# Performance work log

Hardware: AMD Instinct MI355X
Metric: run time of the kernel (lower is better)

Reference implementation:

```python
import jax, jax.numpy as jnp
import numpy as np

NUM_HEADS = 12
HEAD_DIM = 32  # all_head_size(384) / num_heads(12)


def setup_inputs() -> dict:
    key = jax.random.key(0)
    ks = jax.random.split(key, 8)
    B, Sq, Sk, Din, AH = 1, 4096, 4096, 768, 384
    scale = 1.0 / np.sqrt(Din)
    return {
        "hidden_states": jax.random.normal(ks[0], (B, Sq, Din), jnp.float32),
        "encoder_hidden_states": jax.random.normal(ks[1], (B, Sk, Din), jnp.float32),
        "encoder_attention_mask": jnp.zeros((B, 1, 1, Sk), jnp.float32),
        "Wq": jax.random.normal(ks[2], (Din, AH), jnp.float32) * scale,
        "bq": jnp.zeros((AH,), jnp.float32),
        "Wk": jax.random.normal(ks[3], (Din, AH), jnp.float32) * scale,
        "bk": jnp.zeros((AH,), jnp.float32),
        "Wv": jax.random.normal(ks[4], (Din, AH), jnp.float32) * scale,
        "bv": jnp.zeros((AH,), jnp.float32),
    }


def _split_heads(x):
    # [B, S, H*D] -> [B, H, S, D]
    B, S, _ = x.shape
    return x.reshape(B, S, NUM_HEADS, HEAD_DIM).transpose(0, 2, 1, 3)


def reference(hidden_states, encoder_hidden_states, encoder_attention_mask,
              Wq, bq, Wk, bk, Wv, bv):
    q = _split_heads(hidden_states @ Wq + bq)            # [B,H,Sq,D]
    k = _split_heads(encoder_hidden_states @ Wk + bk)    # [B,H,Sk,D]
    v = _split_heads(encoder_hidden_states @ Wv + bv)    # [B,H,Sk,D]

    scores = jnp.einsum('bhqd,bhkd->bhqk', q, k) / np.sqrt(HEAD_DIM)
    scores = scores + encoder_attention_mask              # additive mask, broadcast
    probs = jax.nn.softmax(scores, axis=-1)               # dropout is identity (eval)

    ctx = jnp.einsum('bhqk,bhkd->bhqd', probs, v)         # [B,H,Sq,D]
    B, H, Sq, D = ctx.shape
    return ctx.transpose(0, 2, 1, 3).reshape(B, Sq, H * D)  # [B,Sq,all_head_size]
```

## Files before the change

kernel.cpp:

```cpp
#include <hip/hip_runtime.h>
#include <hip/hip_bf16.h>

#define SQ 4096
#define SKK 4096
#define DIN 768
#define AHS 384
#define NHEAD 12
#define HD 32

typedef __attribute__((ext_vector_type(8))) short bf16x8;
typedef __attribute__((ext_vector_type(4))) float f32x4;
typedef __attribute__((ext_vector_type(4))) unsigned int u32x4;

#define LOG2E 1.4426950408889634f
#define QSCALE 0.25503486168652855f

#define GLD16(gp, lp) __builtin_amdgcn_global_load_lds( \
    (const __attribute__((address_space(1))) void*)(gp), \
    (__attribute__((address_space(3))) void*)(lp), 16, 0, 0)

__device__ __forceinline__ unsigned short bf16_rn(float x){
  unsigned int u = __float_as_uint(x);
  unsigned int r = u + 0x7fffu + ((u>>16)&1u);
  return (unsigned short)(r>>16);
}
__device__ __forceinline__ float bf16_f(unsigned short h){
  return __uint_as_float(((unsigned int)h)<<16);
}
__device__ __forceinline__ float fexp2(float x){
#if __has_builtin(__builtin_amdgcn_exp2f)
  return __builtin_amdgcn_exp2f(x);
#else
  float r; asm("v_exp_f32 %0, %1" : "=v"(r) : "v"(x)); return r;
#endif
}

__global__ void em_kernel(const float* __restrict__ mask, unsigned short* __restrict__ EMB){
  int idx = blockIdx.x*256 + threadIdx.x;
  if (idx < SKK) EMB[idx] = bf16_rn(__expf(mask[idx]));
}

__global__ __launch_bounds__(256) void prep2_kernel(
    const float* __restrict__ Wq, const float* __restrict__ Wk, const float* __restrict__ Wv,
    unsigned short* __restrict__ Wthi, unsigned short* __restrict__ Wtlo)
{
  const int z = blockIdx.z;
  const float* W = (z==0)?Wq:((z==1)?Wk:Wv);
  const int k0 = blockIdx.x*64, n0 = blockIdx.y*64;
  const int tid = threadIdx.x;

  __shared__ float T[64][65];

  const int kr = tid>>2, nc = (tid&3)*16;
  const float* src = W + (size_t)(k0+kr)*AHS + n0 + nc;
  #pragma unroll
  for (int p=0; p<4; ++p){
    f32x4 v = *(const f32x4*)(src + p*4);
    T[kr][nc + p*4 + 0] = v[0];
    T[kr][nc + p*4 + 1] = v[1];
    T[kr][nc + p*4 + 2] = v[2];
    T[kr][nc + p*4 + 3] = v[3];
  }
  __syncthreads();

  const int nr = tid>>2, ks = (tid&3)*16;
  unsigned short* dh = Wthi + (size_t)(z*AHS + n0 + nr)*DIN + k0 + ks;
  unsigned short* dl = Wtlo + (size_t)(z*AHS + n0 + nr)*DIN + k0 + ks;
  #pragma unroll
  for (int half=0; half<2; ++half){
    bf16x8 hv, lv;
    #pragma unroll
    for (int j=0; j<8; ++j){
      float v = T[ks + half*8 + j][nr];
      unsigned short hh = bf16_rn(v);
      hv[j] = (short)hh;
      lv[j] = (short)bf16_rn(v - bf16_f(hh));
    }
    *(bf16x8*)(dh + half*8) = hv;
    *(bf16x8*)(dl + half*8) = lv;
  }
}

__global__ __launch_bounds__(512,2) void proj5_kernel(
    const float* __restrict__ Xh, const float* __restrict__ Xe,
    const unsigned short* __restrict__ Wthi, const unsigned short* __restrict__ Wtlo,
    const float* __restrict__ bq, const float* __restrict__ bk, const float* __restrict__ bv,
    const unsigned short* __restrict__ EMB,
    unsigned short* __restrict__ Qhi, unsigned short* __restrict__ Qlo,
    unsigned short* __restrict__ Khi, unsigned short* __restrict__ Klo,
    unsigned short* __restrict__ Vt)
{
  const int bid = blockIdx.x;
  const int logical = (bid & 7)*36 + (bid >> 3);
  const int mb = logical & 31;
  const int rest = logical >> 5;
  const int nb = rest % 3, z = rest / 3;

  const float* A = (z==0) ? Xh : Xe;
  const unsigned short* Bh = Wthi + (size_t)z*(DIN*AHS);
  const unsigned short* Bl = Wtlo + (size_t)z*(DIN*AHS);
  const float* bias = (z==0) ? bq : ((z==1) ? bk : bv);

  const int m0 = mb*128;
  const int n0 = nb*128;
  const int tid = threadIdx.x;
  const int w = tid>>6, lane = tid&63;
  const int lm = lane&15, g = lane>>4;
  const int wm = w>>1, wn = w&1;

  __shared__ __align__(16) unsigned short SH[32768];

  const int srow = tid>>2, scn = tid&3;
  const int sidx = srow*32 + ((scn ^ ((srow>>1)&3))<<3);
  const float* pA = A + (size_t)(m0 + srow)*DIN + scn*8;
  const size_t gb = (size_t)(n0 + srow)*DIN + scn*8;

  f32x4 xa0, xa1; u32x4 rb, rlb;
  auto sload = [&](int kk){
    xa0 = *(const f32x4*)(pA + kk);
    xa1 = *(const f32x4*)(pA + kk + 4);
    rb  = *(const u32x4*)(Bh + gb + kk);
    if (z != 2) rlb = *(const u32x4*)(Bl + gb + kk);
  };
  auto swrite = [&](int b){
    float xx[8] = {xa0[0],xa0[1],xa0[2],xa0[3],xa1[0],xa1[1],xa1[2],xa1[3]};
    unsigned int hw[4];
    #pragma unroll
    for (int p=0;p<4;++p)
      asm("v_cvt_pk_bf16_f32 %0, %1, %2" : "=v"(hw[p]) : "v"(xx[2*p]), "v"(xx[2*p+1]));
    u32x4 ra = {hw[0],hw[1],hw[2],hw[3]};
    *(u32x4*)&SH[b*16384 + 0*4096 + sidx] = ra;
    *(u32x4*)&SH[b*16384 + 2*4096 + sidx] = rb;
    if (z != 2){
      unsigned int lw[4];
      #pragma unroll
      for (int p=0;p<4;++p){
        float h0 = __uint_as_float(hw[p]<<16);
        float h1 = __uint_as_float(hw[p] & 0xffff0000u);
        float l0 = xx[2*p] - h0, l1 = xx[2*p+1] - h1;
        asm("v_cvt_pk_bf16_f32 %0, %1, %2" : "=v"(lw[p]) : "v"(l0), "v"(l1));
      }
      u32x4 rla = {lw[0],lw[1],lw[2],lw[3]};
      *(u32x4*)&SH[b*16384 + 1*4096 + sidx] = rla;
      *(u32x4*)&SH[b*16384 + 3*4096 + sidx] = rlb;
    }
  };

  f32x4 acc[2][4];
  #pragma unroll
  for (int mi=0;mi<2;++mi)
    #pragma unroll
    for (int ni=0;ni<4;++ni) acc[mi][ni] = (f32x4){0.f,0.f,0.f,0.f};

  auto fidx = [&](int row)->int{ return row*32 + ((g ^ ((row>>1)&3))<<3); };

  sload(0); swrite(0); __syncthreads();
  int cur = 0;

  const int NKS = DIN/32;
  for (int t=0; t<NKS; ++t){
    if (t+1 < NKS) sload((t+1)*32);

    const unsigned short* AhL = &SH[cur*16384 + 0*4096];
    const unsigned short* AlL = &SH[cur*16384 + 1*4096];
    const unsigned short* BhL = &SH[cur*16384 + 2*4096];
    const unsigned short* BlL = &SH[cur*16384 + 3*4096];

    bf16x8 a0h = *(const bf16x8*)&AhL[fidx(wm*32 + lm)];
    bf16x8 a1h = *(const bf16x8*)&AhL[fidx(wm*32 + 16 + lm)];
    bf16x8 a0l, a1l;
    if (z != 2){
      a0l = *(const bf16x8*)&AlL[fidx(wm*32 + lm)];
      a1l = *(const bf16x8*)&AlL[fidx(wm*32 + 16 + lm)];
    }
    __builtin_amdgcn_s_setprio(1);
    #pragma unroll
    for (int ni=0; ni<4; ++ni){
      bf16x8 bh = *(const bf16x8*)&BhL[fidx(wn*64 + ni*16 + lm)];
      acc[0][ni] = __builtin_amdgcn_mfma_f32_16x16x32_bf16(a0h, bh, acc[0][ni], 0,0,0);
      acc[1][ni] = __builtin_amdgcn_mfma_f32_16x16x32_bf16(a1h, bh, acc[1][ni], 0,0,0);
      if (z != 2){
        bf16x8 bl = *(const bf16x8*)&BlL[fidx(wn*64 + ni*16 + lm)];
        acc[0][ni] = __builtin_amdgcn_mfma_f32_16x16x32_bf16(a0h, bl, acc[0][ni], 0,0,0);
        acc[1][ni] = __builtin_amdgcn_mfma_f32_16x16x32_bf16(a1h, bl, acc[1][ni], 0,0,0);
        acc[0][ni] = __builtin_amdgcn_mfma_f32_16x16x32_bf16(a0l, bh, acc[0][ni], 0,0,0);
        acc[1][ni] = __builtin_amdgcn_mfma_f32_16x16x32_bf16(a1l, bh, acc[1][ni], 0,0,0);
      }
    }
    __builtin_amdgcn_s_setprio(0);

    if (t+1 < NKS) swrite(cur^1);
    __syncthreads();
    cur ^= 1;
  }

  if (z != 2){
    #pragma unroll
    for (int ni=0; ni<4; ++ni){
      int col = n0 + wn*64 + ni*16 + lm;
      float bcol = bias[col];
      int hq = col>>5, d = col&31;
      #pragma unroll
      for (int mi=0; mi<2; ++mi){
        #pragma unroll
        for (int r=0; r<4; ++r){
          int row = m0 + wm*32 + mi*16 + g*4 + r;
          float v = acc[mi][ni][r] + bcol;
          if (z==0) v *= QSCALE;
          unsigned short hh = bf16_rn(v);
          unsigned short ll = bf16_rn(v - bf16_f(hh));
          size_t p = (z==0) ? ((size_t)hq*SQ + row)*HD + d
                            : ((size_t)hq*SKK + row)*HD + d;
          if (z==0){ Qhi[p]=hh; Qlo[p]=ll; } else { Khi[p]=hh; Klo[p]=ll; }
        }
      }
    }
  } else {
    #pragma unroll
    for (int ni=0; ni<4; ++ni){
      int lcol = wn*64 + ni*16 + lm;
      float bcol = bias[n0 + lcol];
      #pragma unroll
      for (int mi=0; mi<2; ++mi){
        #pragma unroll
        for (int r=0; r<4; ++r){
          int lrow = wm*32 + mi*16 + g*4 + r;
          float emf = bf16_f(EMB[m0 + lrow]);
          SH[lcol*128 + (lrow ^ ((lcol&7)<<3))] = bf16_rn((acc[mi][ni][r] + bcol) * emf);
        }
      }
    }
    __syncthreads();
    #pragma unroll
    for (int p=0; p<4; ++p){
      int c = tid>>2, rc = (tid&3)*8 + p*32;
      bf16x8 vv = *(const bf16x8*)&SH[c*128 + (rc ^ ((c&7)<<3))];
      *(bf16x8*)(Vt + (size_t)(n0 + c)*SKK + m0 + rc) = vv;
    }
  }
}

__global__ __launch_bounds__(256) void attn_kernel(
    const unsigned short* __restrict__ Qhi, const unsigned short* __restrict__ Qlo,
    const unsigned short* __restrict__ Khi, const unsigned short* __restrict__ Klo,
    const unsigned short* __restrict__ Vt, const unsigned short* __restrict__ EMB,
    float* __restrict__ opart, float* __restrict__ lpart,
    int nkt, int direct, int chunk)
{
  const int bid = blockIdx.x;
  const int logical = (bid & 7)*chunk + (bid >> 3);
  const int qt = logical & 63;
  const int rest = logical >> 6;
  const int h = rest % NHEAD, sp = rest / NHEAD;

  const int tid = threadIdx.x;
  const int w = tid>>6, lane = tid&63;
  const int lm = lane&15, g = lane>>4;
  const int qrow = qt*64 + w*16 + lm;
  const int kbeg = sp*nkt*64;

  __shared__ unsigned short KhL[2][2048];
  __shared__ unsigned short KlL[2][2048];
  __shared__ unsigned short VL [2][2048];

  const int krow_l = 16*w + (lane>>2);
  const int ksw_l = ((krow_l>>1)&1) ^ (((krow_l>>3)&1)<<1);
  const unsigned short* gKh = Khi + (size_t)h*SKK*HD
                            + (size_t)(kbeg + krow_l)*HD + (((lane&3)^ksw_l)<<3);
  const unsigned short* gKl = Klo + (size_t)h*SKK*HD
                            + (size_t)(kbeg + krow_l)*HD + (((lane&3)^ksw_l)<<3);
  const int vrow_l = 8*w + (lane>>3);
  const unsigned short* gV = Vt + (size_t)(h*HD + vrow_l)*SKK + kbeg
                           + (((lane&7)^(lane>>3))<<3);
  const unsigned short* pEM = EMB + kbeg + g*8;

  const int krs = ((lm>>2)<<3) + (lm&3);
  const int rsw = ((krs>>1)&1) ^ (((krs>>3)&1)<<1);
  const int kread0 = krs*32 + ((g ^ rsw)<<3);

  int vr[4];
  vr[0] = (lm*64      + g*8)      ^ ((lm&7)<<3);
  vr[1] = (lm*64      + 32 + g*8) ^ ((lm&7)<<3);
  vr[2] = ((lm+16)*64 + g*8)      ^ ((lm&7)<<3);
  vr[3] = ((lm+16)*64 + 32 + g*8) ^ ((lm&7)<<3);

  bf16x8 qh = *(const bf16x8*)(Qhi + ((size_t)h*SQ + qrow)*HD + g*8);
  bf16x8 ql = *(const bf16x8*)(Qlo + ((size_t)h*SQ + qrow)*HD + g*8);

  f32x4 o0 = {0.f,0.f,0.f,0.f}, o1 = {0.f,0.f,0.f,0.f};
  f32x4 lacc = {0.f,0.f,0.f,0.f};

  GLD16(gKh, &KhL[0][w*512]);
  GLD16(gKl, &KlL[0][w*512]);
  GLD16(gV,  &VL [0][w*512]);
  __syncthreads();

  #pragma unroll 2
  for (int t=0; t<nkt; ++t){
    const int cur = t&1;

    if (t+1 < nkt){
      gKh += 64*HD; gKl += 64*HD; gV += 64;
      GLD16(gKh, &KhL[cur^1][w*512]);
      GLD16(gKl, &KlL[cur^1][w*512]);
      GLD16(gV,  &VL [cur^1][w*512]);
    }

    bf16x8 em0 = *(const bf16x8*)(pEM);
    bf16x8 em1 = *(const bf16x8*)(pEM + 32);
    pEM += 64;

    unsigned int wds[8];
    #pragma unroll
    for (int ks=0; ks<4; ++ks){
      const int kidx = kread0 + (ks&1)*128 + (ks>>1)*1024;
      bf16x8 kh = *(const bf16x8*)(&KhL[cur][kidx]);
      bf16x8 kl = *(const bf16x8*)(&KlL[cur][kidx]);
      f32x4 a = {0.f,0.f,0.f,0.f};
      __builtin_amdgcn_s_setprio(1);
      a = __builtin_amdgcn_mfma_f32_16x16x32_bf16(kh, qh, a, 0,0,0);
      a = __builtin_amdgcn_mfma_f32_16x16x32_bf16(kh, ql, a, 0,0,0);
      a = __builtin_amdgcn_mfma_f32_16x16x32_bf16(kl, qh, a, 0,0,0);
      __builtin_amdgcn_s_setprio(0);
      float p0 = fexp2(a[0]);
      float p1 = fexp2(a[1]);
      float p2 = fexp2(a[2]);
      float p3 = fexp2(a[3]);
      asm("v_cvt_pk_bf16_f32 %0, %1, %2" : "=v"(wds[ks*2])   : "v"(p0), "v"(p1));
      asm("v_cvt_pk_bf16_f32 %0, %1, %2" : "=v"(wds[ks*2+1]) : "v"(p2), "v"(p3));
    }
    u32x4 w0v = {wds[0], wds[1], wds[2], wds[3]};
    u32x4 w1v = {wds[4], wds[5], wds[6], wds[7]};
    bf16x8 pa0 = __builtin_bit_cast(bf16x8, w0v);
    bf16x8 pa1 = __builtin_bit_cast(bf16x8, w1v);

    bf16x8 v00 = *(const bf16x8*)(&VL[cur][vr[0]]);
    bf16x8 v01 = *(const bf16x8*)(&VL[cur][vr[1]]);
    bf16x8 v10 = *(const bf16x8*)(&VL[cur][vr[2]]);
    bf16x8 v11 = *(const bf16x8*)(&VL[cur][vr[3]]);
    __builtin_amdgcn_s_setprio(1);
    o0   = __builtin_amdgcn_mfma_f32_16x16x32_bf16(pa0, v00, o0,   0,0,0);
    o1   = __builtin_amdgcn_mfma_f32_16x16x32_bf16(pa0, v10, o1,   0,0,0);
    lacc = __builtin_amdgcn_mfma_f32_16x16x32_bf16(pa0, em0, lacc, 0,0,0);
    o0   = __builtin_amdgcn_mfma_f32_16x16x32_bf16(pa1, v01, o0,   0,0,0);
    o1   = __builtin_amdgcn_mfma_f32_16x16x32_bf16(pa1, v11, o1,   0,0,0);
    lacc = __builtin_amdgcn_mfma_f32_16x16x32_bf16(pa1, em1, lacc, 0,0,0);
    __builtin_amdgcn_s_setprio(0);

    __syncthreads();
  }

  if (direct){
    #pragma unroll
    for (int r=0;r<4;++r){
      float inv = 1.0f / lacc[r];
      int row = qt*64 + w*16 + g*4 + r;
      opart[(size_t)row*AHS + h*HD + lm]      = o0[r]*inv;
      opart[(size_t)row*AHS + h*HD + 16 + lm] = o1[r]*inv;
    }
  } else {
    #pragma unroll
    for (int r=0;r<4;++r){
      int row = qt*64 + w*16 + g*4 + r;
      opart[((size_t)sp*SQ + row)*AHS + h*HD + lm]      = o0[r];
      opart[((size_t)sp*SQ + row)*AHS + h*HD + 16 + lm] = o1[r];
    }
    if (lm == 0){
      #pragma unroll
      for (int r=0;r<4;++r){
        int row = qt*64 + w*16 + g*4 + r;
        lpart[((size_t)sp*NHEAD + h)*SQ + row] = lacc[r];
      }
    }
  }
}

__global__ void merge_kernel(const float* __restrict__ opart,
                             const float* __restrict__ lpart,
                             float* __restrict__ out, int S){
  int idx = blockIdx.x*256 + threadIdx.x;
  if (idx >= SQ*AHS) return;
  int row = idx/AHS, c = idx - row*AHS;
  int h = c >> 5;
  float num = 0.f, den = 0.f;
  for (int s=0; s<S; ++s){
    num += opart[((size_t)s*SQ + row)*AHS + c];
    den += lpart[((size_t)s*NHEAD + h)*SQ + row];
  }
  out[idx] = num/den;
}

extern "C" void kernel_launch(void* const* d_in, const int* in_sizes, int n_in,
                              void* d_out, int out_size, void* d_ws, size_t ws_size,
                              hipStream_t stream) {
  const float* Xh   = (const float*)d_in[0];
  const float* Xe   = (const float*)d_in[1];
  const float* mask = (const float*)d_in[2];
  const float* Wq   = (const float*)d_in[3];
  const float* bq   = (const float*)d_in[4];
  const float* Wk   = (const float*)d_in[5];
  const float* bk   = (const float*)d_in[6];
  const float* Wv   = (const float*)d_in[7];
  const float* bv   = (const float*)d_in[8];
  float* out = (float*)d_out;

  char* ws = (char*)d_ws;
  auto al256 = [](size_t b)->size_t{ return (b + 255) & ~(size_t)255; };
  size_t off = 0;
  auto alloc = [&](size_t bytes)->void*{ void* p = ws + off; off += al256(bytes); return p; };

  unsigned short* Wthi = (unsigned short*)alloc((size_t)3*DIN*AHS*2);
  unsigned short* Wtlo = (unsigned short*)alloc((size_t)3*DIN*AHS*2);
  unsigned short* EMB  = (unsigned short*)alloc((size_t)SKK*2);
  unsigned short* Qhi  = (unsigned short*)alloc((size_t)NHEAD*SQ*HD*2);
  unsigned short* Qlo  = (unsigned short*)alloc((size_t)NHEAD*SQ*HD*2);
  unsigned short* Khi  = (unsigned short*)alloc((size_t)NHEAD*SKK*HD*2);
  unsigned short* Klo  = (unsigned short*)alloc((size_t)NHEAD*SKK*HD*2);
  unsigned short* Vt   = (unsigned short*)alloc((size_t)AHS*SKK*2);
  const size_t base_end = off;

  const size_t OB = al256((size_t)SQ*AHS*4);
  const size_t MB = al256((size_t)NHEAD*SQ*4);

  auto fits = [&](int S)->bool{
    return base_end + (size_t)S*OB + (size_t)S*MB + 8192 <= ws_size;
  };

  int S = 1, direct = 0;
  if      (fits(4)) S = 4;
  else if (fits(2)) S = 2;
  else if (fits(1)) S = 1;
  else { S = 1; direct = 1; }

  char* ureg = ws + base_end;
  float *opart, *lpart;
  if (!direct){
    opart = (float*)(ureg);
    lpart = (float*)(ureg + (size_t)S*OB);
  } else {
    opart = out; lpart = (float*)ws;
  }

  {
    em_kernel<<<(SKK+255)/256, 256, 0, stream>>>(mask, EMB);
    dim3 grid(DIN/64, AHS/64, 3);
    prep2_kernel<<<grid, 256, 0, stream>>>(Wq, Wk, Wv, Wthi, Wtlo);
  }
  {
    proj5_kernel<<<288, 512, 0, stream>>>(Xh, Xe, Wthi, Wtlo,
                                          bq, bk, bv, EMB, Qhi, Qlo, Khi, Klo, Vt);
  }
  {
    int nblk = 64*NHEAD*S;
    int nkt = (SKK/64)/S;
    attn_kernel<<<nblk, 256, 0, stream>>>(Qhi, Qlo, Khi, Klo, Vt, EMB,
                                          opart, lpart, nkt, direct, nblk/8);
  }
  if (!direct){
    int n = SQ*AHS;
    merge_kernel<<<(n+255)/256, 256, 0, stream>>>(opart, lpart, out, S);
  }
}
```

Before: 113.2 us.

## Stage projection B tiles via direct global-to-LDS loads and halve attention split

In the projection GEMM, the bf16 weight tiles are now loaded with global_load_lds straight into shared memory, using a pre-swizzled source address. This removes the register round trip and the separate LDS store for B, while A is still converted on the fly through registers. The attention key-split factor also drops from 4 to 2. That means fewer partial outputs and a cheaper merge, but the grid gets smaller and each block runs a longer KV loop.

```diff
diff --git a/kernel.cpp b/kernel.cpp
--- a/kernel.cpp
+++ b/kernel.cpp
@@ -81,7 +81,7 @@
   }
 }
 
-__global__ __launch_bounds__(512,2) void proj5_kernel(
+__global__ __launch_bounds__(512,2) void proj7_kernel(
     const float* __restrict__ Xh, const float* __restrict__ Xe,
     const unsigned short* __restrict__ Wthi, const unsigned short* __restrict__ Wtlo,
     const float* __restrict__ bq, const float* __restrict__ bk, const float* __restrict__ bv,
@@ -111,18 +111,22 @@
   __shared__ __align__(16) unsigned short SH[32768];
 
   const int srow = tid>>2, scn = tid&3;
-  const int sidx = srow*32 + ((scn ^ ((srow>>1)&3))<<3);
+  const int swz = (srow>>1)&3;
+  const int sidx = srow*32 + ((scn ^ swz)<<3);
   const float* pA = A + (size_t)(m0 + srow)*DIN + scn*8;
-  const size_t gb = (size_t)(n0 + srow)*DIN + scn*8;
-
-  f32x4 xa0, xa1; u32x4 rb, rlb;
-  auto sload = [&](int kk){
+  const unsigned short* gBh = Bh + (size_t)(n0 + srow)*DIN + ((scn ^ swz)<<3);
+  const unsigned short* gBl = Bl + (size_t)(n0 + srow)*DIN + ((scn ^ swz)<<3);
+
+  f32x4 xa0, xa1;
+  auto sloadA = [&](int kk){
     xa0 = *(const f32x4*)(pA + kk);
     xa1 = *(const f32x4*)(pA + kk + 4);
-    rb  = *(const u32x4*)(Bh + gb + kk);
-    if (z != 2) rlb = *(const u32x4*)(Bl + gb + kk);
   };
-  auto swrite = [&](int b){
+  auto stageB = [&](int b, int kk){
+    GLD16(gBh + kk, &SH[b*16384 + 2*4096 + w*512]);
+    if (z != 2) GLD16(gBl + kk, &SH[b*16384 + 3*4096 + w*512]);
+  };
+  auto swriteA = [&](int b){
     float xx[8] = {xa0[0],xa0[1],xa0[2],xa0[3],xa1[0],xa1[1],xa1[2],xa1[3]};
     unsigned int hw[4];
     #pragma unroll
@@ -130,7 +134,6 @@
       asm("v_cvt_pk_bf16_f32 %0, %1, %2" : "=v"(hw[p]) : "v"(xx[2*p]), "v"(xx[2*p+1]));
     u32x4 ra = {hw[0],hw[1],hw[2],hw[3]};
     *(u32x4*)&SH[b*16384 + 0*4096 + sidx] = ra;
-    *(u32x4*)&SH[b*16384 + 2*4096 + sidx] = rb;
     if (z != 2){
       unsigned int lw[4];
       #pragma unroll
@@ -142,7 +145,6 @@
       }
       u32x4 rla = {lw[0],lw[1],lw[2],lw[3]};
       *(u32x4*)&SH[b*16384 + 1*4096 + sidx] = rla;
-      *(u32x4*)&SH[b*16384 + 3*4096 + sidx] = rlb;
     }
   };
 
@@ -154,12 +156,15 @@
 
   auto fidx = [&](int row)->int{ return row*32 + ((g ^ ((row>>1)&3))<<3); };
 
-  sload(0); swrite(0); __syncthreads();
+  stageB(0, 0); sloadA(0); swriteA(0); __syncthreads();
   int cur = 0;
 
   const int NKS = DIN/32;
   for (int t=0; t<NKS; ++t){
-    if (t+1 < NKS) sload((t+1)*32);
+    if (t+1 < NKS){
+      stageB(cur^1, (t+1)*32);
+      sloadA((t+1)*32);
+    }
 
     const unsigned short* AhL = &SH[cur*16384 + 0*4096];
     const unsigned short* AlL = &SH[cur*16384 + 1*4096];
@@ -189,7 +194,7 @@
     }
     __builtin_amdgcn_s_setprio(0);
 
-    if (t+1 < NKS) swrite(cur^1);
+    if (t+1 < NKS) swriteA(cur^1);
     __syncthreads();
     cur ^= 1;
   }
@@ -427,8 +432,7 @@
   };
 
   int S = 1, direct = 0;
-  if      (fits(4)) S = 4;
-  else if (fits(2)) S = 2;
+  if      (fits(2)) S = 2;
   else if (fits(1)) S = 1;
   else { S = 1; direct = 1; }
 
@@ -447,7 +451,7 @@
     prep2_kernel<<<grid, 256, 0, stream>>>(Wq, Wk, Wv, Wthi, Wtlo);
   }
   {
-    proj5_kernel<<<288, 512, 0, stream>>>(Xh, Xe, Wthi, Wtlo,
+    proj7_kernel<<<288, 512, 0, stream>>>(Xh, Xe, Wthi, Wtlo,
                                           bq, bk, bv, EMB, Qhi, Qlo, Khi, Klo, Vt);
   }
   {
```

Result: no change. 112.6 us (-0.5%).
